# Performance work log

Measured on AMD Instinct MI355X. Metric: run time of the kernel, lower is better.

The kernel has to match this reference:

```python
import jax, jax.numpy as jnp
import numpy as np

B, S, DIM, H = 4, 4096, 2048, 16
HD = DIM // H  # head_dim = 128


def setup_inputs() -> dict:
    key = jax.random.key(0)
    ks = jax.random.split(key, 6)
    X = jax.random.normal(ks[0], (B, S, DIM), dtype=jnp.float32)
    freqs_cos = jax.random.uniform(ks[1], (S, HD), dtype=jnp.float32)
    freqs_sin = jax.random.uniform(ks[2], (S, HD), dtype=jnp.float32)
    attention_mask = jnp.ones((B, S), dtype=jnp.int32)
    # Linear weights stored as [in, out] (equivalent to torch W.T); no bias.
    scale = 0.02
    Wq = jax.random.normal(ks[3], (DIM, DIM), dtype=jnp.float32) * scale
    Wk = jax.random.normal(ks[4], (DIM, DIM), dtype=jnp.float32) * scale
    Wv = jax.random.normal(ks[5], (DIM, DIM), dtype=jnp.float32) * scale
    return {"X": X, "freqs_cos": freqs_cos, "freqs_sin": freqs_sin,
            "attention_mask": attention_mask, "Wq": Wq, "Wk": Wk, "Wv": Wv}


def _rotate_half_interleaved(x):
    # x: [B, S, H, D]; pairs along last dim: (x0, x1) -> (-x1, x0), interleaved
    xp = x.reshape(*x.shape[:-1], HD // 2, 2)
    xt = jnp.stack([-xp[..., 1], xp[..., 0]], axis=-1)
    return xt.reshape(x.shape)


def reference(X, freqs_cos, freqs_sin, attention_mask, Wq, Wk, Wv):
    bs, seq_len, _ = X.shape
    # QKV projections (no bias), fused view to [B, S, H, HD]
    Xq = (X @ Wq).reshape(bs, seq_len, H, HD)
    Xk = (X @ Wk).reshape(bs, seq_len, H, HD)
    Xv = (X @ Wv).reshape(bs, seq_len, H, HD)
    # RoPE: broadcast freqs to (1, S, 1, HD)
    cos = freqs_cos[None, :, None, :]
    sin = freqs_sin[None, :, None, :]
    Xq_out = Xq * cos + _rotate_half_interleaved(Xq) * sin
    Xk_out = Xk * cos + _rotate_half_interleaved(Xk) * sin
    return (Xq_out, Xk_out, Xv)
```

## Files before the change

kernel.cpp:

```cpp
#include <hip/hip_runtime.h>
#include <hip/hip_bf16.h>
#include <stdint.h>

#define B_    4
#define S_    4096
#define DIM_  2048
#define H_    16
#define HD_   128
#define M_    (B_ * S_)
#define K_    DIM_
#define N_    (3 * DIM_)

typedef __attribute__((ext_vector_type(8))) short bf16x8;
typedef __attribute__((ext_vector_type(4))) float f32x4;

__global__ void cvt_x_kernel(const float* __restrict__ X,
                             __hip_bfloat16* __restrict__ Xb) {
    size_t i = ((size_t)blockIdx.x * 256 + threadIdx.x) * 8;
    float4 a = *reinterpret_cast<const float4*>(X + i);
    float4 b = *reinterpret_cast<const float4*>(X + i + 4);
    union { __hip_bfloat16 h[8]; uint4 u; } o;
    o.h[0] = __float2bfloat16(a.x);
    o.h[1] = __float2bfloat16(a.y);
    o.h[2] = __float2bfloat16(a.z);
    o.h[3] = __float2bfloat16(a.w);
    o.h[4] = __float2bfloat16(b.x);
    o.h[5] = __float2bfloat16(b.y);
    o.h[6] = __float2bfloat16(b.z);
    o.h[7] = __float2bfloat16(b.w);
    *reinterpret_cast<uint4*>(Xb + i) = o.u;
}

__global__ void cvt_w_kernel(const float* __restrict__ Wq,
                             const float* __restrict__ Wk,
                             const float* __restrict__ Wv,
                             __hip_bfloat16* __restrict__ Wt) {
    __shared__ float tile[32][33];
    int w = blockIdx.z;
    const float* W = (w == 0) ? Wq : (w == 1) ? Wk : Wv;
    int n0 = blockIdx.x * 32;
    int k0 = blockIdx.y * 32;
    int tx = threadIdx.x, ty = threadIdx.y;
#pragma unroll
    for (int r = 0; r < 4; ++r) {
        int k = k0 + ty + r * 8;
        tile[ty + r * 8][tx] = W[(size_t)k * DIM_ + n0 + tx];
    }
    __syncthreads();
#pragma unroll
    for (int r = 0; r < 4; ++r) {
        int n = n0 + ty + r * 8;
        Wt[(size_t)(w * DIM_ + n) * K_ + k0 + tx] =
            __float2bfloat16(tile[tx][ty + r * 8]);
    }
}

#define BM 256
#define BN 256
#define BK 64
#define NT (K_ / BK)

#define BAR()      asm volatile("s_barrier" ::: "memory")
#define LGKM0()    asm volatile("s_waitcnt lgkmcnt(0)" ::: "memory")
#define WAIT_VM(n) asm volatile("s_waitcnt vmcnt(" #n ")" ::: "memory")

__global__ __launch_bounds__(512, 1) void gemm_rope_kernel(
    const __hip_bfloat16* __restrict__ Xb,
    const __hip_bfloat16* __restrict__ Wt,
    const float* __restrict__ fcos,
    const float* __restrict__ fsin,
    float* __restrict__ out)
{
    __shared__ __hip_bfloat16 As[2][BM * BK];
    __shared__ __hip_bfloat16 Bs[2][BN * BK];

    const int nbn = N_ / BN;
    int bid = blockIdx.x;
    int cpx = gridDim.x >> 3;
    int swz = (bid & 7) * cpx + (bid >> 3);
    int tm = swz / nbn, tn = swz % nbn;
    int m0 = tm * BM, n0 = tn * BN;

    int tid  = threadIdx.x;
    int lane = tid & 63;
    int w    = tid >> 6;
    int wr   = w >> 2;
    int wc   = w & 3;

    int rl   = lane >> 3;
    int gsw  = ((lane & 7) ^ rl) * 8;
    int lcol = (lane & 7) * 8;

    int fr = lane & 15;
    int fq = lane >> 4;
    int l7 = lane & 7;
    int ce0 = ((0 + fq) ^ l7) * 8;
    int ce1 = ((4 + fq) ^ l7) * 8;

#define STAGE_A(t, r) do {                                                     \
        const __hip_bfloat16* _s = Xb + (size_t)(m0 + (r) * 64 + w * 8 + rl) * K_ \
                                      + (t) * BK + gsw;                        \
        __hip_bfloat16* _d = &As[(t) & 1][((r) * 64 + w * 8 + rl) * BK + lcol];\
        __builtin_amdgcn_global_load_lds(                                      \
            (const __attribute__((address_space(1))) void*)_s,                 \
            (__attribute__((address_space(3))) void*)_d, 16, 0, 0);            \
    } while (0)

#define STAGE_B(t, r) do {                                                     \
        const __hip_bfloat16* _s = Wt + (size_t)(n0 + (r) * 64 + w * 8 + rl) * K_ \
                                      + (t) * BK + gsw;                        \
        __hip_bfloat16* _d = &Bs[(t) & 1][((r) * 64 + w * 8 + rl) * BK + lcol];\
        __builtin_amdgcn_global_load_lds(                                      \
            (const __attribute__((address_space(1))) void*)_s,                 \
            (__attribute__((address_space(3))) void*)_d, 16, 0, 0);            \
    } while (0)

    f32x4  acc[2][2][4][2] = {};
    bf16x8 a[4][2];
    bf16x8 b[2][2][2];

#define LDA(buf, qi) do {                                                      \
        _Pragma("unroll")                                                      \
        for (int i = 0; i < 4; ++i) {                                          \
            int _row = wr * 128 + (qi) * 64 + i * 16 + fr;                     \
            a[i][0] = *reinterpret_cast<const bf16x8*>(&As[buf][_row * BK + ce0]); \
            a[i][1] = *reinterpret_cast<const bf16x8*>(&As[buf][_row * BK + ce1]); \
        }                                                                      \
    } while (0)

#define LDB(buf, qj) do {                                                      \
        _Pragma("unroll")                                                      \
        for (int j = 0; j < 2; ++j) {                                          \
            int _row = wc * 64 + (qj) * 32 + j * 16 + fr;                      \
            b[qj][j][0] = *reinterpret_cast<const bf16x8*>(&Bs[buf][_row * BK + ce0]); \
            b[qj][j][1] = *reinterpret_cast<const bf16x8*>(&Bs[buf][_row * BK + ce1]); \
        }                                                                      \
    } while (0)

#define MFMA_Q(qi, qj) do {                                                    \
        __builtin_amdgcn_s_setprio(1);                                         \
        _Pragma("unroll")                                                      \
        for (int i = 0; i < 4; ++i)                                            \
        _Pragma("unroll")                                                      \
        for (int j = 0; j < 2; ++j) {                                          \
            acc[qi][qj][i][j] = __builtin_amdgcn_mfma_f32_16x16x32_bf16(       \
                a[i][0], b[qj][j][0], acc[qi][qj][i][j], 0, 0, 0);             \
            acc[qi][qj][i][j] = __builtin_amdgcn_mfma_f32_16x16x32_bf16(       \
                a[i][1], b[qj][j][1], acc[qi][qj][i][j], 0, 0, 0);             \
        }                                                                      \
        __builtin_amdgcn_s_setprio(0);                                         \
    } while (0)

#pragma unroll
    for (int r = 0; r < 4; ++r) STAGE_A(0, r);
#pragma unroll
    for (int r = 0; r < 4; ++r) STAGE_B(0, r);
#pragma unroll
    for (int r = 0; r < 4; ++r) STAGE_A(1, r);
    WAIT_VM(4);
    BAR();

    for (int t = 0; t < NT; ++t) {
        int buf = t & 1;
        LDA(buf, 0);
        LDB(buf, 0);
        if (t + 1 < NT) { STAGE_B(t + 1, 0); STAGE_B(t + 1, 1); }
        BAR(); LGKM0();
        MFMA_Q(0, 0);
        BAR();
        LDB(buf, 1);
        if (t + 1 < NT) { STAGE_B(t + 1, 2); STAGE_B(t + 1, 3); }
        BAR(); LGKM0();
        MFMA_Q(0, 1);
        BAR();
        LDA(buf, 1);
        BAR(); LGKM0();
        MFMA_Q(1, 0);
        BAR();
        if (t + 2 < NT) {
            STAGE_A(t + 2, 0); STAGE_A(t + 2, 1);
            STAGE_A(t + 2, 2); STAGE_A(t + 2, 3);
        }
        BAR(); LGKM0();
        MFMA_Q(1, 1);
        if (t + 2 < NT) { WAIT_VM(4); } else { WAIT_VM(0); }
        BAR();
    }

#pragma unroll
    for (int qi = 0; qi < 2; ++qi)
#pragma unroll
    for (int i = 0; i < 4; ++i) {
        int mbase = m0 + wr * 128 + qi * 64 + i * 16 + fq * 4;
#pragma unroll
        for (int qj = 0; qj < 2; ++qj)
#pragma unroll
        for (int j = 0; j < 2; ++j) {
            int n = n0 + wc * 64 + qj * 32 + j * 16 + fr;
            int region = n >> 11;
            int cc = n & (DIM_ - 1);
            int d  = cc & (HD_ - 1);
#pragma unroll
            for (int r = 0; r < 4; ++r) {
                int m = mbase + r;
                int s = m & (S_ - 1);
                float g  = acc[qi][qj][i][j][r];
                float gp = __shfl_xor(g, 1, 64);
                float o;
                if (region < 2) {
                    float cv = fcos[s * HD_ + d];
                    float sv = fsin[s * HD_ + d];
                    o = g * cv + ((cc & 1) ? gp * sv : -gp * sv);
                } else {
                    o = g;
                }
                out[(size_t)region * M_ * DIM_ + (size_t)m * DIM_ + cc] = o;
            }
        }
    }
#undef STAGE_A
#undef STAGE_B
#undef LDA
#undef LDB
#undef MFMA_Q
}

extern "C" void kernel_launch(void* const* d_in, const int* in_sizes, int n_in,
                              void* d_out, int out_size, void* d_ws, size_t ws_size,
                              hipStream_t stream) {
    const float* X    = (const float*)d_in[0];
    const float* fcos = (const float*)d_in[1];
    const float* fsin = (const float*)d_in[2];
    const float* Wq   = (const float*)d_in[4];
    const float* Wk   = (const float*)d_in[5];
    const float* Wv   = (const float*)d_in[6];
    float* out = (float*)d_out;

    __hip_bfloat16* Xb = (__hip_bfloat16*)d_ws;
    __hip_bfloat16* Wtp = Xb + (size_t)M_ * K_;

    {
        int threads = 256;
        int blocks = (M_ * K_) / (threads * 8);
        cvt_x_kernel<<<blocks, threads, 0, stream>>>(X, Xb);
    }
    {
        dim3 grid(DIM_ / 32, DIM_ / 32, 3);
        dim3 block(32, 8);
        cvt_w_kernel<<<grid, block, 0, stream>>>(Wq, Wk, Wv, Wtp);
    }
    {
        int blocks = (M_ / BM) * (N_ / BN);
        gemm_rope_kernel<<<blocks, 512, 0, stream>>>(Xb, Wtp, fcos, fsin, out);
    }
}
```

Baseline: 589.9 us.

## Unroll GEMM main loop by two with reworked A/B LDS prefetch schedule

```diff
diff --git a/kernel.cpp b/kernel.cpp
--- a/kernel.cpp
+++ b/kernel.cpp
@@ -59,9 +59,11 @@
 #define BN 256
 #define BK 64
 #define NT (K_ / BK)
+#define NU (NT / 2)
 
 #define BAR()      asm volatile("s_barrier" ::: "memory")
 #define LGKM0()    asm volatile("s_waitcnt lgkmcnt(0)" ::: "memory")
+#define LGKM8()    asm volatile("s_waitcnt lgkmcnt(8)" ::: "memory")
 #define WAIT_VM(n) asm volatile("s_waitcnt vmcnt(" #n ")" ::: "memory")
 
 __global__ __launch_bounds__(512, 1) void gemm_rope_kernel(
@@ -97,19 +99,19 @@
     int ce0 = ((0 + fq) ^ l7) * 8;
     int ce1 = ((4 + fq) ^ l7) * 8;
 
-#define STAGE_A(t, r) do {                                                     \
+#define STAGE_A(t, bb, r) do {                                                 \
         const __hip_bfloat16* _s = Xb + (size_t)(m0 + (r) * 64 + w * 8 + rl) * K_ \
                                       + (t) * BK + gsw;                        \
-        __hip_bfloat16* _d = &As[(t) & 1][((r) * 64 + w * 8 + rl) * BK + lcol];\
+        __hip_bfloat16* _d = &As[bb][((r) * 64 + w * 8 + rl) * BK + lcol];     \
         __builtin_amdgcn_global_load_lds(                                      \
             (const __attribute__((address_space(1))) void*)_s,                 \
             (__attribute__((address_space(3))) void*)_d, 16, 0, 0);            \
     } while (0)
 
-#define STAGE_B(t, r) do {                                                     \
+#define STAGE_B(t, bb, r) do {                                                 \
         const __hip_bfloat16* _s = Wt + (size_t)(n0 + (r) * 64 + w * 8 + rl) * K_ \
                                       + (t) * BK + gsw;                        \
-        __hip_bfloat16* _d = &Bs[(t) & 1][((r) * 64 + w * 8 + rl) * BK + lcol];\
+        __hip_bfloat16* _d = &Bs[bb][((r) * 64 + w * 8 + rl) * BK + lcol];     \
         __builtin_amdgcn_global_load_lds(                                      \
             (const __attribute__((address_space(1))) void*)_s,                 \
             (__attribute__((address_space(3))) void*)_d, 16, 0, 0);            \
@@ -119,21 +121,21 @@
     bf16x8 a[4][2];
     bf16x8 b[2][2][2];
 
-#define LDA(buf, qi) do {                                                      \
+#define LDA(bb, qi) do {                                                       \
         _Pragma("unroll")                                                      \
         for (int i = 0; i < 4; ++i) {                                          \
             int _row = wr * 128 + (qi) * 64 + i * 16 + fr;                     \
-            a[i][0] = *reinterpret_cast<const bf16x8*>(&As[buf][_row * BK + ce0]); \
-            a[i][1] = *reinterpret_cast<const bf16x8*>(&As[buf][_row * BK + ce1]); \
+            a[i][0] = *reinterpret_cast<const bf16x8*>(&As[bb][_row * BK + ce0]); \
+            a[i][1] = *reinterpret_cast<const bf16x8*>(&As[bb][_row * BK + ce1]); \
         }                                                                      \
     } while (0)
 
-#define LDB(buf, qj) do {                                                      \
+#define LDB(bb, qj) do {                                                       \
         _Pragma("unroll")                                                      \
         for (int j = 0; j < 2; ++j) {                                          \
             int _row = wc * 64 + (qj) * 32 + j * 16 + fr;                      \
-            b[qj][j][0] = *reinterpret_cast<const bf16x8*>(&Bs[buf][_row * BK + ce0]); \
-            b[qj][j][1] = *reinterpret_cast<const bf16x8*>(&Bs[buf][_row * BK + ce1]); \
+            b[qj][j][0] = *reinterpret_cast<const bf16x8*>(&Bs[bb][_row * BK + ce0]); \
+            b[qj][j][1] = *reinterpret_cast<const bf16x8*>(&Bs[bb][_row * BK + ce1]); \
         }                                                                      \
     } while (0)
 
@@ -152,38 +154,58 @@
     } while (0)
 
 #pragma unroll
-    for (int r = 0; r < 4; ++r) STAGE_A(0, r);
-#pragma unroll
-    for (int r = 0; r < 4; ++r) STAGE_B(0, r);
-#pragma unroll
-    for (int r = 0; r < 4; ++r) STAGE_A(1, r);
+    for (int r = 0; r < 4; ++r) STAGE_A(0, 0, r);
+#pragma unroll
+    for (int r = 0; r < 4; ++r) STAGE_B(0, 0, r);
+#pragma unroll
+    for (int r = 0; r < 4; ++r) STAGE_B(1, 1, r);
     WAIT_VM(4);
     BAR();
 
-    for (int t = 0; t < NT; ++t) {
-        int buf = t & 1;
-        LDA(buf, 0);
-        LDB(buf, 0);
-        if (t + 1 < NT) { STAGE_B(t + 1, 0); STAGE_B(t + 1, 1); }
+    for (int u = 0; u < NU; ++u) {
+        int T0 = 2 * u, T1 = 2 * u + 1;
+        bool last = (u == NU - 1);
+        LDA(0, 0); LDB(0, 0);
+        STAGE_A(T1, 1, 0); STAGE_A(T1, 1, 1);
+        LGKM8();
         BAR(); LGKM0();
         MFMA_Q(0, 0);
         BAR();
-        LDB(buf, 1);
-        if (t + 1 < NT) { STAGE_B(t + 1, 2); STAGE_B(t + 1, 3); }
+        LDB(0, 1);
+        STAGE_A(T1, 1, 2); STAGE_A(T1, 1, 3);
         BAR(); LGKM0();
         MFMA_Q(0, 1);
         BAR();
-        LDA(buf, 1);
+        LDA(0, 1);
+        if (!last) { STAGE_B(T0 + 2, 0, 0); STAGE_B(T0 + 2, 0, 1); }
         BAR(); LGKM0();
         MFMA_Q(1, 0);
         BAR();
-        if (t + 2 < NT) {
-            STAGE_A(t + 2, 0); STAGE_A(t + 2, 1);
-            STAGE_A(t + 2, 2); STAGE_A(t + 2, 3);
-        }
-        BAR(); LGKM0();
+        if (!last) { STAGE_A(T0 + 2, 0, 0); STAGE_A(T0 + 2, 0, 1); }
+        BAR();
         MFMA_Q(1, 1);
-        if (t + 2 < NT) { WAIT_VM(4); } else { WAIT_VM(0); }
+        if (last) { WAIT_VM(0); } else { WAIT_VM(4); }
+        BAR();
+        LDA(1, 0); LDB(1, 0);
+        if (!last) { STAGE_A(T0 + 2, 0, 2); STAGE_A(T0 + 2, 0, 3); }
+        LGKM8();
+        BAR(); LGKM0();
+        MFMA_Q(0, 0);
+        BAR();
+        LDB(1, 1);
+        if (!last) { STAGE_B(T0 + 2, 0, 2); STAGE_B(T0 + 2, 0, 3); }
+        BAR(); LGKM0();
+        MFMA_Q(0, 1);
+        BAR();
+        LDA(1, 1);
+        if (!last) { STAGE_B(T1 + 2, 1, 0); STAGE_B(T1 + 2, 1, 1); }
+        BAR(); LGKM0();
+        MFMA_Q(1, 0);
+        BAR();
+        if (!last) { STAGE_B(T1 + 2, 1, 2); STAGE_B(T1 + 2, 1, 3); }
+        BAR();
+        MFMA_Q(1, 1);
+        if (!last) { WAIT_VM(4); }
         BAR();
     }
 
@@ -236,7 +258,7 @@
     const float* Wv   = (const float*)d_in[6];
     float* out = (float*)d_out;
 
-    __hip_bfloat16* Xb = (__hip_bfloat16*)d_ws;
+    __hip_bfloat16* Xb  = (__hip_bfloat16*)d_ws;
     __hip_bfloat16* Wtp = Xb + (size_t)M_ * K_;
 
     {
```

Result: faster. 572.9 us (-2.9%).
